# Kernel optimization log

Hardware: AMD Instinct MI355X
Metric: run time of the kernel (lower is better)

Reference implementation:

```python
import jax, jax.numpy as jnp
import numpy as np

NHEAD = 16
DHEAD = 128  # dim_embed // nhead
ROPE_BASE = 10000.0


def rmsnorm(x, g):
    eps = jnp.finfo(x.dtype).eps  # torch nn.RMSNorm default eps=None -> dtype eps
    return x * jax.lax.rsqrt(jnp.mean(x * x, axis=-1, keepdims=True) + eps) * g


def rope(x):
    # torchtune-style interleaved RoPE. x: [B,S,H,D]
    B, S, H, D = x.shape
    freqs = 1.0 / (ROPE_BASE ** (jnp.arange(0, D, 2, dtype=jnp.float32) / D))  # [D/2]
    ang = jnp.arange(S, dtype=jnp.float32)[:, None] * freqs[None, :]           # [S,D/2]
    cos = jnp.cos(ang)[None, :, None, :]
    sin = jnp.sin(ang)[None, :, None, :]
    x1, x2 = x[..., 0::2], x[..., 1::2]
    return jnp.stack([x1 * cos - x2 * sin, x1 * sin + x2 * cos], axis=-1).reshape(B, S, H, D)


def setup_inputs() -> dict:
    key = jax.random.key(0)
    B, S, E, C = 4, 2048, 2048, 512
    ks = jax.random.split(key, 9)
    std = 0.02
    h = jax.random.normal(ks[0], (B, S, E), jnp.float32)
    w_d_kv = jax.random.normal(ks[1], (C, E), jnp.float32) * std
    w_u_k = jax.random.normal(ks[2], (E, C), jnp.float32) * std
    w_u_v = jax.random.normal(ks[3], (E, C), jnp.float32) * std
    w_d_q = jax.random.normal(ks[4], (C, E), jnp.float32) * std
    w_u_q = jax.random.normal(ks[5], (E, C), jnp.float32) * std
    w_kr = jax.random.normal(ks[6], (E, E), jnp.float32) * std
    w_qr = jax.random.normal(ks[7], (E, C), jnp.float32) * std
    w_o = jax.random.normal(ks[8], (E, E), jnp.float32) * std
    g1 = jnp.ones((C,), jnp.float32)
    g2 = jnp.ones((C,), jnp.float32)
    g3 = jnp.ones((E,), jnp.float32)
    return {"h": h, "w_d_kv": w_d_kv, "w_u_k": w_u_k, "w_u_v": w_u_v,
            "w_d_q": w_d_q, "w_u_q": w_u_q, "w_kr": w_kr, "w_qr": w_qr,
            "w_o": w_o, "g1": g1, "g2": g2, "g3": g3}


def reference(h, w_d_kv, w_u_k, w_u_v, w_d_q, w_u_q, w_kr, w_qr, w_o, g1, g2, g3):
    # Eval (inference) path of MLA with absorbed weights; no kv/kr cache.
    B, S, E = h.shape
    cq = rmsnorm(h @ w_d_q.T, g1)          # [B,S,C]
    ckv = rmsnorm(h @ w_d_kv.T, g2)        # [B,S,C]
    qr = rope((cq @ w_qr.T).reshape(B, S, NHEAD, DHEAD)).reshape(B, S, E)
    kr = rope((h @ w_kr.T).reshape(B, S, NHEAD, DHEAD)).reshape(B, S, E)
    # absorbed_w_q = (w_d_q.T @ w_u_q.T) @ w_u_k : [E,C]
    absorbed_w_q = (w_d_q.T @ w_u_q.T) @ w_u_k
    # absorbed_w_o = w_u_v.T @ w_o.T : [C,E]
    absorbed_w_o = w_u_v.T @ w_o.T
    aq = h @ absorbed_w_q                  # [B,S,C]  (note: raw h, as in source)
    scores = jnp.einsum('bsc,btc->bst', aq, ckv) + jnp.einsum('bse,bte->bst', qr, kr)
    attn = jax.nn.softmax(scores / np.float32(np.sqrt(NHEAD + DHEAD)), axis=-1)
    o = jnp.einsum('bst,btc->bsc', attn, ckv)
    u = rmsnorm(o @ absorbed_w_o, g3)      # [B,S,E]
    return (u, ckv, kr)
```

## Files before the change

kernel.cpp:

```cpp
#include <hip/hip_runtime.h>
#include <stdint.h>

typedef __attribute__((ext_vector_type(8))) short bf16x8;
typedef __attribute__((ext_vector_type(8))) unsigned short u16x8;
typedef __attribute__((ext_vector_type(4))) float floatx4;

__device__ __forceinline__ uint16_t f2bf(float f) {
  union { float f; uint32_t u; } v; v.f = f;
  uint32_t r = v.u + 0x7fffu + ((v.u >> 16) & 1u);
  return (uint16_t)(r >> 16);
}
__device__ __forceinline__ float bf2f(uint16_t b) {
  union { uint32_t u; float f; } v; v.u = ((uint32_t)b) << 16;
  return v.f;
}
__device__ __forceinline__ float ld_as_float(float v) { return v; }
__device__ __forceinline__ float ld_as_float(uint16_t v) { return bf2f(v); }

__device__ __forceinline__ void mfma16(floatx4& d, bf16x8 a, bf16x8 b) {
  asm("v_mfma_f32_16x16x32_bf16 %0, %1, %2, %0" : "+v"(d) : "v"(a), "v"(b));
}

#define FENCE() asm volatile("" ::: "memory")
#define SCHED() __builtin_amdgcn_sched_barrier(0)
#define SBAR()                                  \
  do {                                          \
    FENCE();                                    \
    __builtin_amdgcn_sched_barrier(0);          \
    __builtin_amdgcn_s_barrier();               \
    __builtin_amdgcn_sched_barrier(0);          \
    FENCE();                                    \
  } while (0)

template<int MODE>
__global__ void __launch_bounds__(512, 1) gemm256v3(
    const uint16_t* __restrict__ A, const uint16_t* __restrict__ B,
    void* __restrict__ C0v, void* __restrict__ C1v, void* __restrict__ C2v,
    int K, int lda, int ldb, int ldc,
    long sA, long sB, long sC, int swzG)
{
  __shared__ __attribute__((aligned(16))) char lds[131072];
  const int tid = threadIdx.x;
  const int w = tid >> 6, l = tid & 63;
  const int wm = w >> 2, wn = w & 3;

  const int gx = gridDim.x;
  const int nwg = gx * gridDim.y;
  int id = blockIdx.y * gx + blockIdx.x;
  if ((nwg & 7) == 0) id = (id & 7) * (nwg >> 3) + (id >> 3);
  const int grp = gx * swzG;
  const int ing = id % grp;
  const long bm = (long)(ing / swzG) * 256;
  const long bn = ((long)(id / grp) * swzG + (ing % swzG)) * 256;
  A += (long)blockIdx.z * sA;
  B += (long)blockIdx.z * sB;

  const int scol = (((l & 3) ^ ((l >> 3) & 3)) << 3);
  const uint16_t* gA = A + (bm + w * 16 + (l >> 2)) * (long)lda + scol;
  const uint16_t* gB = B + (bn + w * 16 + (l >> 2)) * (long)ldb + scol;
  const int ldsw = w * 1024;

#define STG_A3(slot, k0, r)                                                    \
  __builtin_amdgcn_global_load_lds(gA + (k0) + (long)(r) * 128 * lda,          \
      (uint16_t*)(lds + (slot) * 32768 + (r) * 8192 + ldsw), 16, 0, 0)
#define STG_B3(slot, k0, r)                                                    \
  __builtin_amdgcn_global_load_lds(gB + (k0) + (long)(r) * 128 * ldb,          \
      (uint16_t*)(lds + (slot) * 32768 + 16384 + (r) * 8192 + ldsw), 16, 0, 0)

  const int lr = l & 15;
  const int chunkx = (((l >> 4) ^ ((lr >> 1) & 3)) << 4);
  const int aoff = (wm * 128 + lr) * 64 + chunkx;
  const int boff = 16384 + (wn * 64 + lr) * 64 + chunkx;

  floatx4 acc[8][4];
#pragma unroll
  for (int i = 0; i < 8; i++)
#pragma unroll
    for (int j = 0; j < 4; j++) acc[i][j] = (floatx4){0.f, 0.f, 0.f, 0.f};

  const int nt = K >> 5;
#pragma unroll
  for (int tt = 0; tt < 3; tt++) {
    STG_A3(tt, tt * 32, 0); STG_A3(tt, tt * 32, 1);
    STG_B3(tt, tt * 32, 0); STG_B3(tt, tt * 32, 1);
  }
  asm volatile("s_waitcnt vmcnt(8)" ::: "memory");
  SBAR();

  bf16x8 Bf[4], Bfn[4], Af0[4], Af1[4];
#pragma unroll
  for (int j = 0; j < 4; j++) Bf[j] = *(const bf16x8*)(lds + boff + j * 1024);
#pragma unroll
  for (int i = 0; i < 4; i++) Af0[i] = *(const bf16x8*)(lds + aoff + i * 1024);

  for (int t = 0; t < nt; t++) {
    const char* Ls = lds + (t & 3) * 32768;
    const char* Ln = lds + ((t + 1) & 3) * 32768;
    const long pk0 = (long)(t + 3) << 5;
    const int pslot = (t + 3) & 3;
    const bool pf = (t + 3 < nt);

#pragma unroll
    for (int i = 0; i < 4; i++) Af1[i] = *(const bf16x8*)(Ls + aoff + (4 + i) * 1024);
    SCHED();
    if (pf) { STG_A3(pslot, pk0, 0); STG_A3(pslot, pk0, 1); }
    asm volatile("s_waitcnt lgkmcnt(4)" ::: "memory");
    SCHED();
    __builtin_amdgcn_s_setprio(1);
#pragma unroll
    for (int i = 0; i < 4; i++)
#pragma unroll
      for (int j = 0; j < 4; j++) mfma16(acc[i][j], Af0[i], Bf[j]);
    __builtin_amdgcn_s_setprio(0);
    SCHED();

    if (t + 3 < nt)      asm volatile("s_waitcnt vmcnt(6)" ::: "memory");
    else if (t + 2 < nt) asm volatile("s_waitcnt vmcnt(4)" ::: "memory");
    else if (t + 1 < nt) asm volatile("s_waitcnt vmcnt(0)" ::: "memory");
    asm volatile("s_waitcnt lgkmcnt(0)" ::: "memory");
    SBAR();

    if (t + 1 < nt) {
#pragma unroll
      for (int j = 0; j < 4; j++) Bfn[j] = *(const bf16x8*)(Ln + boff + j * 1024);
#pragma unroll
      for (int i = 0; i < 4; i++) Af0[i] = *(const bf16x8*)(Ln + aoff + i * 1024);
    }
    SCHED();
    if (pf) { STG_B3(pslot, pk0, 0); STG_B3(pslot, pk0, 1); }
    SCHED();
    __builtin_amdgcn_s_setprio(1);
#pragma unroll
    for (int i = 0; i < 4; i++)
#pragma unroll
      for (int j = 0; j < 4; j++) mfma16(acc[4 + i][j], Af1[i], Bf[j]);
    __builtin_amdgcn_s_setprio(0);
    SCHED();
#pragma unroll
    for (int j = 0; j < 4; j++) Bf[j] = Bfn[j];
  }
#undef STG_A3
#undef STG_B3

  const long crow = bm + wm * 128 + ((l >> 4) * 4);
  const long ccol = bn + wn * 64 + (l & 15);
  if constexpr (MODE == 0) {
    float* C = (float*)C0v + (long)blockIdx.z * sC;
#pragma unroll
    for (int i = 0; i < 8; i++)
#pragma unroll
      for (int r = 0; r < 4; r++) {
        long row = crow + i * 16 + r;
#pragma unroll
        for (int j = 0; j < 4; j++) C[row * (long)ldc + ccol + j * 16] = acc[i][j][r];
      }
  } else if constexpr (MODE == 1) {
    uint16_t* C = (uint16_t*)C0v + (long)blockIdx.z * sC;
#pragma unroll
    for (int i = 0; i < 8; i++)
#pragma unroll
      for (int r = 0; r < 4; r++) {
        long row = crow + i * 16 + r;
#pragma unroll
        for (int j = 0; j < 4; j++) C[row * (long)ldc + ccol + j * 16] = f2bf(acc[i][j][r]);
      }
  } else if constexpr (MODE == 3) {
    const float s = 1.0f / 12.0f;
    uint16_t* C = (uint16_t*)C0v + (long)blockIdx.z * sC;
#pragma unroll
    for (int i = 0; i < 8; i++)
#pragma unroll
      for (int r = 0; r < 4; r++) {
        long row = crow + i * 16 + r;
#pragma unroll
        for (int j = 0; j < 4; j++) C[row * (long)ldc + ccol + j * 16] = f2bf(acc[i][j][r] * s);
      }
  } else if constexpr (MODE == 4 || MODE == 5) {
    const float2* __restrict__ tab = (const float2*)C1v;
    uint16_t* Cb = (uint16_t*)C0v;
    float* Cf = (float*)C2v;
    const float sgn = (l & 1) ? 1.0f : -1.0f;
#pragma unroll
    for (int i = 0; i < 8; i++)
#pragma unroll
      for (int r = 0; r < 4; r++) {
        long row = crow + i * 16 + r;
        const float2* trow = tab + (((int)(row & 2047)) << 6);
#pragma unroll
        for (int j = 0; j < 4; j++) {
          long c = ccol + j * 16;
          float v = acc[i][j][r];
          float pp = __shfl_xor(v, 1);
          float2 cs = trow[((int)(c & 127)) >> 1];
          float y = v * cs.x + sgn * pp * cs.y;
          Cb[row * 2560 + 512 + c] = f2bf(y);
          if constexpr (MODE == 5) Cf[row * 2048 + c] = y;
        }
      }
  } else {
    if (bn < 512) {
      uint16_t* C = (uint16_t*)C0v;
#pragma unroll
      for (int i = 0; i < 8; i++)
#pragma unroll
        for (int r = 0; r < 4; r++) {
          long row = crow + i * 16 + r;
#pragma unroll
          for (int j = 0; j < 4; j++) C[row * 512 + ccol + j * 16] = f2bf(acc[i][j][r]);
        }
    } else if (bn < 1024) {
      float* C = (float*)C1v;
      const long cc = ccol - 512;
#pragma unroll
      for (int i = 0; i < 8; i++)
#pragma unroll
        for (int r = 0; r < 4; r++) {
          long row = crow + i * 16 + r;
#pragma unroll
          for (int j = 0; j < 4; j++) C[row * 512 + cc + j * 16] = acc[i][j][r];
        }
    } else {
      uint16_t* C = (uint16_t*)C2v;
      const long cc = ccol - 1024;
#pragma unroll
      for (int i = 0; i < 8; i++)
#pragma unroll
        for (int r = 0; r < 4; r++) {
          long row = crow + i * 16 + r;
#pragma unroll
          for (int j = 0; j < 4; j++) C[row * 2560 + cc + j * 16] = f2bf(acc[i][j][r]);
        }
    }
  }
}

template<int OUTB>
__global__ void __launch_bounds__(512, 2) gemm256(
    const uint16_t* __restrict__ A, const uint16_t* __restrict__ B,
    void* __restrict__ Cv, int K, int lda, int ldb, int ldc,
    long sA, long sB, long sC)
{
  __shared__ __attribute__((aligned(16))) char lds[147456];
  const int tid = threadIdx.x;
  const int w = tid >> 6, l = tid & 63;
  const int wm = w >> 1, wn = w & 1;

  const int gx = gridDim.x;
  const int nwg = gx * gridDim.y;
  int id = blockIdx.y * gx + blockIdx.x;
  if ((nwg & 7) == 0) id = (id & 7) * (nwg >> 3) + (id >> 3);
  const long bm = (long)(id % gx) * 256;
  const long bn = (long)(id / gx) * 128;
  A += (long)blockIdx.z * sA;
  B += (long)blockIdx.z * sB;

  const int sr = l >> 3;
  const int sc = l & 7;
  const int scol = ((sc ^ sr) << 3);
  const uint16_t* gA = A + (bm + w * 8 + sr) * (long)lda + scol;
  const uint16_t* gB = B + (bn + w * 8 + sr) * (long)ldb + scol;
  const int ldsw = w * 1024;

#define STAGE_A(bufi, k0, r)                                                     \
  __builtin_amdgcn_global_load_lds(gA + (k0) + (long)(r) * 64 * lda,             \
      (uint16_t*)(lds + (bufi) * 49152 + (r) * 8192 + ldsw), 16, 0, 0)
#define STAGE_B(bufi, k0, r)                                                     \
  __builtin_amdgcn_global_load_lds(gB + (k0) + (long)(r) * 64 * ldb,             \
      (uint16_t*)(lds + (bufi) * 49152 + 32768 + (r) * 8192 + ldsw), 16, 0, 0)

  const int lr = l & 15;
  const int kk = (l >> 4) << 4;
  const int msk = (l & 7) << 4;
  const int ko0 = kk ^ msk;
  const int ko1 = (64 + kk) ^ msk;
  const int arow = (wm * 64 + lr) * 128;
  const int brow = (wn * 64 + lr) * 128;

  floatx4 acc[4][4];
#pragma unroll
  for (int i = 0; i < 4; i++)
#pragma unroll
    for (int j = 0; j < 4; j++) acc[i][j] = (floatx4){0.f, 0.f, 0.f, 0.f};

  const int nt = K >> 6;
#pragma unroll
  for (int r = 0; r < 4; r++) STAGE_A(0, 0, r);
#pragma unroll
  for (int r = 0; r < 2; r++) STAGE_B(0, 0, r);
#pragma unroll
  for (int r = 0; r < 4; r++) STAGE_A(1, 64, r);
#pragma unroll
  for (int r = 0; r < 2; r++) STAGE_B(1, 64, r);
  asm volatile("s_waitcnt vmcnt(6)" ::: "memory");
  SBAR();

  bf16x8 af0[4], bf0[4], af1[4], bf1[4];
  {
    const char* LA = lds + arow;
    const char* LB = lds + 32768 + brow;
#pragma unroll
    for (int i = 0; i < 4; i++) af0[i] = *(const bf16x8*)(LA + i * 2048 + ko0);
#pragma unroll
    for (int j = 0; j < 4; j++) bf0[j] = *(const bf16x8*)(LB + j * 2048 + ko0);
  }

  for (int t = 0; t < nt; t++) {
    const int buf = t % 3;
    const int pbuf = (t + 2) % 3;
    const long pk0 = (long)(t + 2) << 6;
    const char* LA = lds + buf * 49152 + arow;
    const char* LB = lds + buf * 49152 + 32768 + brow;
    const bool pf = (t + 2 < nt);

    if (pf) { STAGE_A(pbuf, pk0, 0); STAGE_A(pbuf, pk0, 1); STAGE_B(pbuf, pk0, 0); }
#pragma unroll
    for (int i = 0; i < 4; i++) af1[i] = *(const bf16x8*)(LA + i * 2048 + ko1);
#pragma unroll
    for (int j = 0; j < 4; j++) bf1[j] = *(const bf16x8*)(LB + j * 2048 + ko1);
    SCHED();
    __builtin_amdgcn_s_setprio(1);
#pragma unroll
    for (int i = 0; i < 4; i++)
#pragma unroll
      for (int j = 0; j < 4; j++) mfma16(acc[i][j], af0[i], bf0[j]);
    __builtin_amdgcn_s_setprio(0);
    SCHED();

    if (pf) { STAGE_A(pbuf, pk0, 2); STAGE_A(pbuf, pk0, 3); STAGE_B(pbuf, pk0, 1); }
    if (t < nt - 2) asm volatile("s_waitcnt vmcnt(6) lgkmcnt(0)" ::: "memory");
    else            asm volatile("s_waitcnt vmcnt(0) lgkmcnt(0)" ::: "memory");
    SBAR();
    if (t < nt - 1) {
      const char* LAn = lds + ((t + 1) % 3) * 49152 + arow;
      const char* LBn = lds + ((t + 1) % 3) * 49152 + 32768 + brow;
#pragma unroll
      for (int i = 0; i < 4; i++) af0[i] = *(const bf16x8*)(LAn + i * 2048 + ko0);
#pragma unroll
      for (int j = 0; j < 4; j++) bf0[j] = *(const bf16x8*)(LBn + j * 2048 + ko0);
    }
    SCHED();
    __builtin_amdgcn_s_setprio(1);
#pragma unroll
    for (int i = 0; i < 4; i++)
#pragma unroll
      for (int j = 0; j < 4; j++) mfma16(acc[i][j], af1[i], bf1[j]);
    __builtin_amdgcn_s_setprio(0);
    SCHED();
  }
#undef STAGE_A
#undef STAGE_B

  const long crow = bm + wm * 64 + ((l >> 4) * 4);
  const long ccol = bn + wn * 64 + (l & 15);
  if constexpr (OUTB == 0) {
    float* C = (float*)Cv + (long)blockIdx.z * sC;
#pragma unroll
    for (int i = 0; i < 4; i++)
#pragma unroll
      for (int r = 0; r < 4; r++) {
        long row = crow + i * 16 + r;
#pragma unroll
        for (int j = 0; j < 4; j++) C[row * (long)ldc + ccol + j * 16] = acc[i][j][r];
      }
  } else {
    uint16_t* C = (uint16_t*)Cv + (long)blockIdx.z * sC;
#pragma unroll
    for (int i = 0; i < 4; i++)
#pragma unroll
      for (int r = 0; r < 4; r++) {
        long row = crow + i * 16 + r;
#pragma unroll
        for (int j = 0; j < 4; j++) C[row * (long)ldc + ccol + j * 16] = f2bf(acc[i][j][r]);
      }
  }
}

template<int OUTB>
__global__ void __launch_bounds__(256) gemm_bt(
    const uint16_t* __restrict__ A, const uint16_t* __restrict__ B,
    void* __restrict__ Cv, int K, int lda, int ldb, int ldc,
    long sA, long sB, long sC)
{
  __shared__ alignas(16) uint16_t As[4096];
  __shared__ alignas(16) uint16_t Bs[4096];
  const int tid = threadIdx.x;
  const int w = tid >> 6, l = tid & 63;
  const int wr = w >> 1, wc = w & 1;
  const long bm = (long)blockIdx.x * 128, bn = (long)blockIdx.y * 128;
  A += (long)blockIdx.z * sA;
  B += (long)blockIdx.z * sB;

  const uint16_t* ga0 = A + (bm + w * 16 + (l >> 2)) * (long)lda + (l & 3) * 8;
  const uint16_t* ga1 = ga0 + 64L * lda;
  const uint16_t* gb0 = B + (bn + w * 16 + (l >> 2)) * (long)ldb + (l & 3) * 8;
  const uint16_t* gb1 = gb0 + 64L * ldb;
  uint16_t* la0 = &As[w * 512];
  uint16_t* la1 = &As[2048 + w * 512];
  uint16_t* lb0 = &Bs[w * 512];
  uint16_t* lb1 = &Bs[2048 + w * 512];

  floatx4 acc[4][4];
#pragma unroll
  for (int i = 0; i < 4; i++)
#pragma unroll
    for (int j = 0; j < 4; j++) acc[i][j] = (floatx4){0.f, 0.f, 0.f, 0.f};

  const int rA = (wr * 64 + (l & 15)) * 32 + (l >> 4) * 8;
  const int rB = (wc * 64 + (l & 15)) * 32 + (l >> 4) * 8;

  for (int k0 = 0; k0 < K; k0 += 32) {
    __builtin_amdgcn_global_load_lds(ga0, la0, 16, 0, 0);
    __builtin_amdgcn_global_load_lds(ga1, la1, 16, 0, 0);
    __builtin_amdgcn_global_load_lds(gb0, lb0, 16, 0, 0);
    __builtin_amdgcn_global_load_lds(gb1, lb1, 16, 0, 0);
    ga0 += 32; ga1 += 32; gb0 += 32; gb1 += 32;
    __syncthreads();
    bf16x8 af[4], bfr[4];
#pragma unroll
    for (int i = 0; i < 4; i++) af[i] = *(const bf16x8*)&As[rA + i * 512];
#pragma unroll
    for (int j = 0; j < 4; j++) bfr[j] = *(const bf16x8*)&Bs[rB + j * 512];
#pragma unroll
    for (int i = 0; i < 4; i++)
#pragma unroll
      for (int j = 0; j < 4; j++) mfma16(acc[i][j], af[i], bfr[j]);
    __syncthreads();
  }

  const long crow = bm + wr * 64 + ((l >> 4) * 4);
  const long ccol = bn + wc * 64 + (l & 15);
  if constexpr (OUTB == 0) {
    float* C = (float*)Cv + (long)blockIdx.z * sC;
#pragma unroll
    for (int i = 0; i < 4; i++)
#pragma unroll
      for (int r = 0; r < 4; r++) {
        long row = crow + i * 16 + r;
#pragma unroll
        for (int j = 0; j < 4; j++) C[row * (long)ldc + ccol + j * 16] = acc[i][j][r];
      }
  } else {
    uint16_t* C = (uint16_t*)Cv + (long)blockIdx.z * sC;
#pragma unroll
    for (int i = 0; i < 4; i++)
#pragma unroll
      for (int r = 0; r < 4; r++) {
        long row = crow + i * 16 + r;
#pragma unroll
        for (int j = 0; j < 4; j++) C[row * (long)ldc + ccol + j * 16] = f2bf(acc[i][j][r]);
      }
  }
}

__global__ void __launch_bounds__(256) reduceK(const float* __restrict__ in,
                                               uint16_t* __restrict__ out,
                                               long n, int S, long stride) {
  long i = ((long)blockIdx.x * 256 + threadIdx.x) * 4;
  if (i >= n) return;
  float4 s = *(const float4*)(in + i);
  for (int k = 1; k < S; k++) {
    float4 t = *(const float4*)(in + k * stride + i);
    s.x += t.x; s.y += t.y; s.z += t.z; s.w += t.w;
  }
  ushort4 o; o.x = f2bf(s.x); o.y = f2bf(s.y); o.z = f2bf(s.z); o.w = f2bf(s.w);
  *(ushort4*)(out + i) = o;
}

__global__ void __launch_bounds__(256) prep_all(
    const float* __restrict__ h,
    const float* __restrict__ wdq, const float* __restrict__ wdkv,
    const float* __restrict__ wqr, const float* __restrict__ wkr,
    const float* __restrict__ wo,
    uint16_t* __restrict__ hb,
    uint16_t* __restrict__ wdq_b, uint16_t* __restrict__ wdkv_b,
    uint16_t* __restrict__ wqr_b, uint16_t* __restrict__ wkr_b,
    uint16_t* __restrict__ wo_b, float2* __restrict__ rtab)
{
  const int b = blockIdx.x;
  if (b < 27648) {
    const float* src; uint16_t* dst; long off;
    if (b < 16384)      { src = h;    dst = hb;     off = b; }
    else if (b < 17408) { src = wdq;  dst = wdq_b;  off = b - 16384; }
    else if (b < 18432) { src = wdkv; dst = wdkv_b; off = b - 17408; }
    else if (b < 19456) { src = wqr;  dst = wqr_b;  off = b - 18432; }
    else if (b < 23552) { src = wkr;  dst = wkr_b;  off = b - 19456; }
    else                { src = wo;   dst = wo_b;   off = b - 23552; }
    long i = (off * 256 + threadIdx.x) * 4;
    float4 v = *(const float4*)(src + i);
    ushort4 o; o.x = f2bf(v.x); o.y = f2bf(v.y); o.z = f2bf(v.z); o.w = f2bf(v.w);
    *(ushort4*)(dst + i) = o;
  } else {
    int idx = (b - 27648) * 256 + threadIdx.x;
    int s = idx >> 6, fi = idx & 63;
    float f = powf(10000.0f, -(float)fi * (1.0f / 64.0f));
    float ang = (float)s * f;
    rtab[idx] = make_float2(cosf(ang), sinf(ang));
  }
}

__global__ void __launch_bounds__(256) transpose4(
    const float* __restrict__ wuk, const float* __restrict__ wuq,
    const float* __restrict__ wuv, const float* __restrict__ wdq,
    uint16_t* __restrict__ wukT, uint16_t* __restrict__ wuqT,
    uint16_t* __restrict__ wuvT, uint16_t* __restrict__ wdqT)
{
  __shared__ float tile[32][33];
  const int bt = blockIdx.x;
  const float* in; uint16_t* out; int ld_in, ld_out, rb, cb;
  if (bt < 3072) {
    const int op = bt >> 10, rem = bt & 1023;
    in = (op == 0) ? wuk : (op == 1) ? wuq : wuv;
    out = (op == 0) ? wukT : (op == 1) ? wuqT : wuvT;
    ld_in = 512; ld_out = 2048;
    cb = (rem & 15) * 32; rb = (rem >> 4) * 32;
  } else {
    const int rem = bt - 3072;
    in = wdq; out = wdqT; ld_in = 2048; ld_out = 512;
    cb = (rem & 63) * 32; rb = (rem >> 6) * 32;
  }
#pragma unroll
  for (int i = 0; i < 32; i += 8)
    tile[threadIdx.y + i][threadIdx.x] =
        in[(long)(rb + threadIdx.y + i) * ld_in + cb + threadIdx.x];
  __syncthreads();
#pragma unroll
  for (int i = 0; i < 32; i += 8)
    out[(long)(cb + threadIdx.y + i) * ld_out + rb + threadIdx.x] =
        f2bf(tile[threadIdx.x][threadIdx.y + i]);
}

template<typename TIN>
__global__ void __launch_bounds__(256) transpose_to_bf16(
    const TIN* __restrict__ in, uint16_t* __restrict__ out,
    int ld_in, int ld_out, long sIn, long sOut)
{
  __shared__ float tile[32][33];
  in += (long)blockIdx.z * sIn;
  out += (long)blockIdx.z * sOut;
  const int rb = blockIdx.y * 32, cb = blockIdx.x * 32;
#pragma unroll
  for (int i = 0; i < 32; i += 8)
    tile[threadIdx.y + i][threadIdx.x] =
        ld_as_float(in[(long)(rb + threadIdx.y + i) * ld_in + cb + threadIdx.x]);
  __syncthreads();
#pragma unroll
  for (int i = 0; i < 32; i += 8)
    out[(long)(cb + threadIdx.y + i) * ld_out + rb + threadIdx.x] =
        f2bf(tile[threadIdx.x][threadIdx.y + i]);
}

template<int PT, typename TIN>
__global__ void __launch_bounds__(256) rmsnorm_k(
    const TIN* __restrict__ in, const float* __restrict__ g,
    float* __restrict__ out_f, uint16_t* __restrict__ out_b, int ld_b)
{
  constexpr int DIM = PT * 256;
  __shared__ float sm[9];
  const TIN* x = in + (long)blockIdx.x * DIM;
  const int base = threadIdx.x * PT;
  float v[PT];
  if constexpr (sizeof(TIN) == 2) {
    if constexpr (PT >= 8) {
#pragma unroll
      for (int i = 0; i < PT; i += 8) {
        u16x8 t = *(const u16x8*)&x[base + i];
#pragma unroll
        for (int q = 0; q < 8; q++) v[i + q] = bf2f(t[q]);
      }
    } else {
#pragma unroll
      for (int i = 0; i < PT; i += 2) {
        ushort2 t = *(const ushort2*)&x[base + i];
        v[i] = bf2f(t.x); v[i + 1] = bf2f(t.y);
      }
    }
  } else if constexpr (PT == 2) {
    float2 t = *(const float2*)&x[base]; v[0] = t.x; v[1] = t.y;
  } else {
#pragma unroll
    for (int i = 0; i < PT; i += 4) {
      float4 t = *(const float4*)&x[base + i];
      v[i] = t.x; v[i + 1] = t.y; v[i + 2] = t.z; v[i + 3] = t.w;
    }
  }
  float ss = 0.f;
#pragma unroll
  for (int i = 0; i < PT; i++) ss += v[i] * v[i];
#pragma unroll
  for (int o = 32; o; o >>= 1) ss += __shfl_down(ss, o);
  if ((threadIdx.x & 63) == 0) sm[threadIdx.x >> 6] = ss;
  __syncthreads();
  if (threadIdx.x == 0)
    sm[8] = rsqrtf((sm[0] + sm[1] + sm[2] + sm[3]) * (1.0f / DIM) + 1.1920929e-7f);
  __syncthreads();
  const float sc = sm[8];
#pragma unroll
  for (int i = 0; i < PT; i++) {
    float y = v[i] * sc * g[base + i];
    if (out_f) out_f[(long)blockIdx.x * DIM + base + i] = y;
    if (out_b) out_b[(long)blockIdx.x * ld_b + base + i] = f2bf(y);
  }
}

__global__ void __launch_bounds__(256) softmax_k(const uint16_t* __restrict__ sc,
                                                 uint16_t* __restrict__ attn) {
  __shared__ float sm[9];
  const uint16_t* x = sc + ((long)blockIdx.x << 11);
  const int base = threadIdx.x * 8;
  float v[8];
  u16x8 t = *(const u16x8*)&x[base];
#pragma unroll
  for (int i = 0; i < 8; i++) v[i] = bf2f(t[i]);
  float m = -1e30f;
#pragma unroll
  for (int i = 0; i < 8; i++) m = fmaxf(m, v[i]);
#pragma unroll
  for (int o = 32; o; o >>= 1) m = fmaxf(m, __shfl_down(m, o));
  if ((threadIdx.x & 63) == 0) sm[threadIdx.x >> 6] = m;
  __syncthreads();
  if (threadIdx.x == 0)
    sm[8] = fmaxf(fmaxf(sm[0], sm[1]), fmaxf(sm[2], sm[3]));
  __syncthreads();
  m = sm[8];
  __syncthreads();
  float ss = 0.f;
#pragma unroll
  for (int i = 0; i < 8; i++) { v[i] = __expf(v[i] - m); ss += v[i]; }
#pragma unroll
  for (int o = 32; o; o >>= 1) ss += __shfl_down(ss, o);
  if ((threadIdx.x & 63) == 0) sm[threadIdx.x >> 6] = ss;
  __syncthreads();
  if (threadIdx.x == 0) sm[8] = 1.0f / (sm[0] + sm[1] + sm[2] + sm[3]);
  __syncthreads();
  const float r = sm[8];
  ushort4 o1, o2;
  o1.x = f2bf(v[0] * r); o1.y = f2bf(v[1] * r); o1.z = f2bf(v[2] * r); o1.w = f2bf(v[3] * r);
  o2.x = f2bf(v[4] * r); o2.y = f2bf(v[5] * r); o2.z = f2bf(v[6] * r); o2.w = f2bf(v[7] * r);
  uint16_t* dst = attn + ((long)blockIdx.x << 11) + base;
  *(ushort4*)dst = o1;
  *(ushort4*)(dst + 4) = o2;
}

extern "C" void kernel_launch(void* const* d_in, const int* in_sizes, int n_in,
                              void* d_out, int out_size, void* d_ws, size_t ws_size,
                              hipStream_t stream) {
  (void)in_sizes; (void)n_in; (void)out_size; (void)ws_size;
  const float* h    = (const float*)d_in[0];
  const float* wdkv = (const float*)d_in[1];
  const float* wuk  = (const float*)d_in[2];
  const float* wuv  = (const float*)d_in[3];
  const float* wdq  = (const float*)d_in[4];
  const float* wuq  = (const float*)d_in[5];
  const float* wkr  = (const float*)d_in[6];
  const float* wqr  = (const float*)d_in[7];
  const float* wo   = (const float*)d_in[8];
  const float* g1   = (const float*)d_in[9];
  const float* g2   = (const float*)d_in[10];
  const float* g3   = (const float*)d_in[11];

  float* u_out   = (float*)d_out;
  float* ckv_out = u_out + 16777216L;
  float* kr_out  = ckv_out + 4194304L;

  char* p = (char*)d_ws;
  auto alloc = [&](size_t bytes) -> void* {
    void* q = (void*)p; p += (bytes + 255) & ~(size_t)255; return q;
  };
  uint16_t* hb     = (uint16_t*)alloc(16777216ULL * 2);
  uint16_t* wcat   = (uint16_t*)alloc(3145728ULL * 2);
  uint16_t* wqr_b  = (uint16_t*)alloc(1048576ULL * 2);
  uint16_t* wkr_b  = (uint16_t*)alloc(4194304ULL * 2);
  uint16_t* wo_b   = (uint16_t*)alloc(4194304ULL * 2);
  uint16_t* wukT   = (uint16_t*)alloc(1048576ULL * 2);
  uint16_t* wuqT   = (uint16_t*)alloc(1048576ULL * 2);
  uint16_t* wuvT   = (uint16_t*)alloc(1048576ULL * 2);
  uint16_t* wdqT   = (uint16_t*)alloc(1048576ULL * 2);
  uint16_t* T1t    = (uint16_t*)alloc(262144ULL * 2);
  uint16_t* awoT   = (uint16_t*)alloc(1048576ULL * 2);
  uint16_t* cqpre  = (uint16_t*)alloc(4194304ULL * 2);
  uint16_t* cq_b   = (uint16_t*)alloc(4194304ULL * 2);
  uint16_t* catq   = (uint16_t*)alloc(20971520ULL * 2);
  uint16_t* catk   = (uint16_t*)alloc(20971520ULL * 2);
  uint16_t* ckvT   = (uint16_t*)alloc(4194304ULL * 2);
  uint16_t* o_b    = (uint16_t*)alloc(4194304ULL * 2);
  float2*   rtab   = (float2*)alloc(131072ULL * 8);
  float*    tmpS2  = (float*)alloc(4194304ULL * 4);
  float*    tmpB   = (float*)alloc(16777216ULL * 4);
  float*    redT   = (float*)alloc(1048576ULL * 4);
  float*    redW   = (float*)alloc(4194304ULL * 4);
  uint16_t* tmpBb  = (uint16_t*)tmpB;
  uint16_t* attn   = catq;

  uint16_t* wdq_b  = wcat;
  uint16_t* wdkv_b = wcat + 1048576;
  uint16_t* Bqt    = wcat + 2097152;

  const dim3 b256(256);
  const dim3 b512(512);
  const dim3 tb(32, 8);

  prep_all<<<dim3(28160), b256, 0, stream>>>(
      h, wdq, wdkv, wqr, wkr, wo, hb, wdq_b, wdkv_b, wqr_b, wkr_b, wo_b, rtab);
  transpose4<<<dim3(4096), tb, 0, stream>>>(
      wuk, wuq, wuv, wdq, wukT, wuqT, wuvT, wdqT);

  gemm_bt<0><<<dim3(4, 4, 4), b256, 0, stream>>>(
      wukT, wuqT, redT, 512, 2048, 2048, 512, 512L, 512L, 262144L);
  reduceK<<<dim3(256), b256, 0, stream>>>(redT, T1t, 262144L, 4, 262144L);
  gemm_bt<0><<<dim3(16, 4, 4), b256, 0, stream>>>(
      wo_b, wuvT, redW, 512, 2048, 2048, 512, 512L, 512L, 1048576L);
  reduceK<<<dim3(1024), b256, 0, stream>>>(redW, awoT, 1048576L, 4, 1048576L);
  gemm_bt<1><<<dim3(4, 16, 1), b256, 0, stream>>>(T1t, wdqT, Bqt, 512, 512, 512, 2048, 0, 0, 0);

  gemm256v3<2><<<dim3(32, 6, 1), b512, 0, stream>>>(
      hb, wcat, cqpre, tmpS2, catq, 2048, 2048, 2048, 0, 0, 0, 0, 2);
  rmsnorm_k<2, uint16_t><<<dim3(8192), b256, 0, stream>>>(cqpre, g1, nullptr, cq_b, 512);
  gemm256v3<4><<<dim3(32, 8, 1), b512, 0, stream>>>(
      cq_b, wqr_b, catq, rtab, nullptr, 512, 512, 512, 2560, 0, 0, 0, 4);
  rmsnorm_k<2, float><<<dim3(8192), b256, 0, stream>>>(tmpS2, g2, ckv_out, catk, 2560);
  transpose_to_bf16<uint16_t><<<dim3(16, 64, 4), tb, 0, stream>>>(
      catk, ckvT, 2560, 2048, 2048L * 2560, 512L * 2048);
  gemm256v3<5><<<dim3(32, 8, 1), b512, 0, stream>>>(
      hb, wkr_b, catk, rtab, kr_out, 2048, 2048, 2048, 2560, 0, 0, 0, 4);
  gemm256v3<3><<<dim3(8, 8, 4), b512, 0, stream>>>(
      catq, catk, tmpBb, nullptr, nullptr, 2560, 2560, 2560, 2048,
      5242880L, 5242880L, 4194304L, 2);
  softmax_k<<<dim3(8192), b256, 0, stream>>>(tmpBb, attn);
  gemm256<1><<<dim3(8, 4, 4), b512, 0, stream>>>(
      attn, ckvT, o_b, 2048, 2048, 2048, 512, 4194304L, 1048576L, 1048576L);
  gemm256v3<1><<<dim3(32, 8, 1), b512, 0, stream>>>(
      o_b, awoT, tmpBb, nullptr, nullptr, 512, 512, 512, 2048, 0, 0, 0, 4);
  rmsnorm_k<8, uint16_t><<<dim3(8192), b256, 0, stream>>>(tmpBb, g3, u_out, nullptr, 0);
}
```

Baseline: 472.2 us.

## Fold RMSNorm gain into weights and per-row scale into GEMM epilogue

```diff
diff --git a/kernel.cpp b/kernel.cpp
--- a/kernel.cpp
+++ b/kernel.cpp
@@ -178,7 +178,8 @@
   } else if constexpr (MODE == 4 || MODE == 5) {
     const float2* __restrict__ tab = (const float2*)C1v;
     uint16_t* Cb = (uint16_t*)C0v;
-    float* Cf = (float*)C2v;
+    const float* __restrict__ S = (MODE == 4) ? (const float*)C2v : nullptr;
+    float* Cf = (MODE == 5) ? (float*)C2v : nullptr;
     const float sgn = (l & 1) ? 1.0f : -1.0f;
 #pragma unroll
     for (int i = 0; i < 8; i++)
@@ -186,10 +187,13 @@
       for (int r = 0; r < 4; r++) {
         long row = crow + i * 16 + r;
         const float2* trow = tab + (((int)(row & 2047)) << 6);
+        float srow = 1.0f;
+        if constexpr (MODE == 4) srow = S ? S[row] : 1.0f;
 #pragma unroll
         for (int j = 0; j < 4; j++) {
           long c = ccol + j * 16;
           float v = acc[i][j][r];
+          if constexpr (MODE == 4) v *= srow;
           float pp = __shfl_xor(v, 1);
           float2 cs = trow[((int)(c & 127)) >> 1];
           float y = v * cs.x + sgn * pp * cs.y;
@@ -470,63 +474,69 @@
     const float* __restrict__ h,
     const float* __restrict__ wdq, const float* __restrict__ wdkv,
     const float* __restrict__ wqr, const float* __restrict__ wkr,
-    const float* __restrict__ wo,
+    const float* __restrict__ wo, const float* __restrict__ g1,
+    const float* __restrict__ wuk, const float* __restrict__ wuq,
+    const float* __restrict__ wuv,
     uint16_t* __restrict__ hb,
     uint16_t* __restrict__ wdq_b, uint16_t* __restrict__ wdkv_b,
     uint16_t* __restrict__ wqr_b, uint16_t* __restrict__ wkr_b,
-    uint16_t* __restrict__ wo_b, float2* __restrict__ rtab)
+    uint16_t* __restrict__ wo_b, float2* __restrict__ rtab,
+    uint16_t* __restrict__ wukT, uint16_t* __restrict__ wuqT,
+    uint16_t* __restrict__ wuvT, uint16_t* __restrict__ wdqT)
 {
   const int b = blockIdx.x;
   if (b < 27648) {
+    if (b >= 18432 && b < 19456) {
+      long i = ((long)(b - 18432) * 256 + threadIdx.x) * 4;
+      float4 v = *(const float4*)(wqr + i);
+      int c = (int)(i & 511);
+      float4 g = *(const float4*)(g1 + c);
+      ushort4 o;
+      o.x = f2bf(v.x * g.x); o.y = f2bf(v.y * g.y);
+      o.z = f2bf(v.z * g.z); o.w = f2bf(v.w * g.w);
+      *(ushort4*)(wqr_b + i) = o;
+      return;
+    }
     const float* src; uint16_t* dst; long off;
     if (b < 16384)      { src = h;    dst = hb;     off = b; }
     else if (b < 17408) { src = wdq;  dst = wdq_b;  off = b - 16384; }
     else if (b < 18432) { src = wdkv; dst = wdkv_b; off = b - 17408; }
-    else if (b < 19456) { src = wqr;  dst = wqr_b;  off = b - 18432; }
     else if (b < 23552) { src = wkr;  dst = wkr_b;  off = b - 19456; }
     else                { src = wo;   dst = wo_b;   off = b - 23552; }
     long i = (off * 256 + threadIdx.x) * 4;
     float4 v = *(const float4*)(src + i);
     ushort4 o; o.x = f2bf(v.x); o.y = f2bf(v.y); o.z = f2bf(v.z); o.w = f2bf(v.w);
     *(ushort4*)(dst + i) = o;
-  } else {
+  } else if (b < 28160) {
     int idx = (b - 27648) * 256 + threadIdx.x;
     int s = idx >> 6, fi = idx & 63;
     float f = powf(10000.0f, -(float)fi * (1.0f / 64.0f));
     float ang = (float)s * f;
     rtab[idx] = make_float2(cosf(ang), sinf(ang));
-  }
-}
-
-__global__ void __launch_bounds__(256) transpose4(
-    const float* __restrict__ wuk, const float* __restrict__ wuq,
-    const float* __restrict__ wuv, const float* __restrict__ wdq,
-    uint16_t* __restrict__ wukT, uint16_t* __restrict__ wuqT,
-    uint16_t* __restrict__ wuvT, uint16_t* __restrict__ wdqT)
-{
-  __shared__ float tile[32][33];
-  const int bt = blockIdx.x;
-  const float* in; uint16_t* out; int ld_in, ld_out, rb, cb;
-  if (bt < 3072) {
-    const int op = bt >> 10, rem = bt & 1023;
-    in = (op == 0) ? wuk : (op == 1) ? wuq : wuv;
-    out = (op == 0) ? wukT : (op == 1) ? wuqT : wuvT;
-    ld_in = 512; ld_out = 2048;
-    cb = (rem & 15) * 32; rb = (rem >> 4) * 32;
   } else {
-    const int rem = bt - 3072;
-    in = wdq; out = wdqT; ld_in = 2048; ld_out = 512;
-    cb = (rem & 63) * 32; rb = (rem >> 6) * 32;
-  }
-#pragma unroll
-  for (int i = 0; i < 32; i += 8)
-    tile[threadIdx.y + i][threadIdx.x] =
-        in[(long)(rb + threadIdx.y + i) * ld_in + cb + threadIdx.x];
-  __syncthreads();
-#pragma unroll
-  for (int i = 0; i < 32; i += 8)
-    out[(long)(cb + threadIdx.y + i) * ld_out + rb + threadIdx.x] =
-        f2bf(tile[threadIdx.x][threadIdx.y + i]);
+    __shared__ float tile[32][33];
+    const int bt = b - 28160;
+    const int tx = threadIdx.x & 31, ty = threadIdx.x >> 5;
+    const float* in; uint16_t* out; int ld_in, ld_out, rb, cb;
+    if (bt < 3072) {
+      const int op = bt >> 10, rem = bt & 1023;
+      in = (op == 0) ? wuk : (op == 1) ? wuq : wuv;
+      out = (op == 0) ? wukT : (op == 1) ? wuqT : wuvT;
+      ld_in = 512; ld_out = 2048;
+      cb = (rem & 15) * 32; rb = (rem >> 4) * 32;
+    } else {
+      const int rem = bt - 3072;
+      in = wdq; out = wdqT; ld_in = 2048; ld_out = 512;
+      cb = (rem & 63) * 32; rb = (rem >> 6) * 32;
+    }
+#pragma unroll
+    for (int i = 0; i < 32; i += 8)
+      tile[ty + i][tx] = in[(long)(rb + ty + i) * ld_in + cb + tx];
+    __syncthreads();
+#pragma unroll
+    for (int i = 0; i < 32; i += 8)
+      out[(long)(cb + ty + i) * ld_out + rb + tx] = f2bf(tile[tx][ty + i]);
+  }
 }
 
 template<typename TIN>
@@ -547,6 +557,43 @@
   for (int i = 0; i < 32; i += 8)
     out[(long)(cb + threadIdx.y + i) * ld_out + rb + threadIdx.x] =
         f2bf(tile[threadIdx.x][threadIdx.y + i]);
+}
+
+__global__ void __launch_bounds__(256) norm_pair(
+    const uint16_t* __restrict__ cqpre, float* __restrict__ sVec,
+    const float* __restrict__ ckvpre, const float* __restrict__ g2,
+    float* __restrict__ ckv_out, uint16_t* __restrict__ catk)
+{
+  __shared__ float sm[9];
+  const int b = blockIdx.x;
+  const int base = threadIdx.x * 2;
+  float v0, v1;
+  if (b < 8192) {
+    ushort2 t = *(const ushort2*)&cqpre[(long)b * 512 + base];
+    v0 = bf2f(t.x); v1 = bf2f(t.y);
+  } else {
+    float2 t = *(const float2*)&ckvpre[(long)(b - 8192) * 512 + base];
+    v0 = t.x; v1 = t.y;
+  }
+  float ss = v0 * v0 + v1 * v1;
+#pragma unroll
+  for (int o = 32; o; o >>= 1) ss += __shfl_down(ss, o);
+  if ((threadIdx.x & 63) == 0) sm[threadIdx.x >> 6] = ss;
+  __syncthreads();
+  if (threadIdx.x == 0)
+    sm[8] = rsqrtf((sm[0] + sm[1] + sm[2] + sm[3]) * (1.0f / 512.0f) + 1.1920929e-7f);
+  __syncthreads();
+  const float sc = sm[8];
+  if (b < 8192) {
+    if (threadIdx.x == 0) sVec[b] = sc;
+  } else {
+    const long row = b - 8192;
+    float y0 = v0 * sc * g2[base];
+    float y1 = v1 * sc * g2[base + 1];
+    *(float2*)&ckv_out[row * 512 + base] = make_float2(y0, y1);
+    ushort2 o; o.x = f2bf(y0); o.y = f2bf(y1);
+    *(ushort2*)&catk[row * 2560 + base] = o;
+  }
 }
 
 template<int PT, typename TIN>
@@ -560,22 +607,12 @@
   const int base = threadIdx.x * PT;
   float v[PT];
   if constexpr (sizeof(TIN) == 2) {
-    if constexpr (PT >= 8) {
-#pragma unroll
-      for (int i = 0; i < PT; i += 8) {
-        u16x8 t = *(const u16x8*)&x[base + i];
-#pragma unroll
-        for (int q = 0; q < 8; q++) v[i + q] = bf2f(t[q]);
-      }
-    } else {
-#pragma unroll
-      for (int i = 0; i < PT; i += 2) {
-        ushort2 t = *(const ushort2*)&x[base + i];
-        v[i] = bf2f(t.x); v[i + 1] = bf2f(t.y);
-      }
+#pragma unroll
+    for (int i = 0; i < PT; i += 8) {
+      u16x8 t = *(const u16x8*)&x[base + i];
+#pragma unroll
+      for (int q = 0; q < 8; q++) v[i + q] = bf2f(t[q]);
     }
-  } else if constexpr (PT == 2) {
-    float2 t = *(const float2*)&x[base]; v[0] = t.x; v[1] = t.y;
   } else {
 #pragma unroll
     for (int i = 0; i < PT; i += 4) {
@@ -678,7 +715,7 @@
   uint16_t* T1t    = (uint16_t*)alloc(262144ULL * 2);
   uint16_t* awoT   = (uint16_t*)alloc(1048576ULL * 2);
   uint16_t* cqpre  = (uint16_t*)alloc(4194304ULL * 2);
-  uint16_t* cq_b   = (uint16_t*)alloc(4194304ULL * 2);
+  float*    sVec   = (float*)alloc(8192ULL * 4);
   uint16_t* catq   = (uint16_t*)alloc(20971520ULL * 2);
   uint16_t* catk   = (uint16_t*)alloc(20971520ULL * 2);
   uint16_t* ckvT   = (uint16_t*)alloc(4194304ULL * 2);
@@ -699,10 +736,9 @@
   const dim3 b512(512);
   const dim3 tb(32, 8);
 
-  prep_all<<<dim3(28160), b256, 0, stream>>>(
-      h, wdq, wdkv, wqr, wkr, wo, hb, wdq_b, wdkv_b, wqr_b, wkr_b, wo_b, rtab);
-  transpose4<<<dim3(4096), tb, 0, stream>>>(
-      wuk, wuq, wuv, wdq, wukT, wuqT, wuvT, wdqT);
+  prep_all<<<dim3(32256), b256, 0, stream>>>(
+      h, wdq, wdkv, wqr, wkr, wo, g1, wuk, wuq, wuv,
+      hb, wdq_b, wdkv_b, wqr_b, wkr_b, wo_b, rtab, wukT, wuqT, wuvT, wdqT);
 
   gemm_bt<0><<<dim3(4, 4, 4), b256, 0, stream>>>(
       wukT, wuqT, redT, 512, 2048, 2048, 512, 512L, 512L, 262144L);
@@ -714,10 +750,9 @@
 
   gemm256v3<2><<<dim3(32, 6, 1), b512, 0, stream>>>(
       hb, wcat, cqpre, tmpS2, catq, 2048, 2048, 2048, 0, 0, 0, 0, 2);
-  rmsnorm_k<2, uint16_t><<<dim3(8192), b256, 0, stream>>>(cqpre, g1, nullptr, cq_b, 512);
+  norm_pair<<<dim3(16384), b256, 0, stream>>>(cqpre, sVec, tmpS2, g2, ckv_out, catk);
   gemm256v3<4><<<dim3(32, 8, 1), b512, 0, stream>>>(
-      cq_b, wqr_b, catq, rtab, nullptr, 512, 512, 512, 2560, 0, 0, 0, 4);
-  rmsnorm_k<2, float><<<dim3(8192), b256, 0, stream>>>(tmpS2, g2, ckv_out, catk, 2560);
+      cqpre, wqr_b, catq, rtab, sVec, 512, 512, 512, 2560, 0, 0, 0, 4);
   transpose_to_bf16<uint16_t><<<dim3(16, 64, 4), tb, 0, stream>>>(
       catk, ckvT, 2560, 2048, 2048L * 2560, 512L * 2048);
   gemm256v3<5><<<dim3(32, 8, 1), b512, 0, stream>>>(
```

Result: faster. 462.8 us (-2.0%).
